# Performance work log

Measured on AMD Instinct MI355X. Metric: run time of the kernel, lower is better.

The kernel has to match this reference:

```python
import jax, jax.numpy as jnp
import numpy as np

B, N, IN_DIM, HEADS, PER_HEAD = 8, 512, 256, 4, 32
OUT_DIM = HEADS * PER_HEAD  # 128
NEG_SLOPE = 0.2


def setup_inputs() -> dict:
    key = jax.random.key(0)
    ks = jax.random.split(key, 8)
    x = jax.random.normal(ks[0], (B, N, IN_DIM), jnp.float32)
    adj = jax.random.randint(ks[1], (B, N, N), 0, 2, jnp.int32)
    sl = 1.0 / np.sqrt(IN_DIM)
    W_l = jax.random.normal(ks[2], (IN_DIM, OUT_DIM), jnp.float32) * sl  # source proj
    b_l = jnp.zeros((OUT_DIM,), jnp.float32)
    W_r = jax.random.normal(ks[3], (IN_DIM, OUT_DIM), jnp.float32) * sl  # target proj
    b_r = jnp.zeros((OUT_DIM,), jnp.float32)
    att = jax.random.normal(ks[4], (HEADS, PER_HEAD), jnp.float32) * (1.0 / np.sqrt(PER_HEAD))
    bias = jnp.zeros((OUT_DIM,), jnp.float32)
    return {"x": x, "adj": adj, "W_l": W_l, "b_l": b_l, "W_r": W_r, "b_r": b_r,
            "att": att, "bias": bias}


def _gatv2_single(x_b, adj_b, W_l, b_l, W_r, b_r, att, bias):
    # PyG GATv2Conv: remove_self_loops + add_self_loops -> diagonal forced to 1
    n = x_b.shape[0]
    adj_sl = jnp.fill_diagonal(adj_b, 1, inplace=False)
    # edge_index = adj.nonzero().t(): source = row, target = col
    m = (adj_sl != 0).T  # m[i, j]: source j feeds target i
    xl = (x_b @ W_l + b_l).reshape(n, HEADS, PER_HEAD)  # source-side features
    xr = (x_b @ W_r + b_r).reshape(n, HEADS, PER_HEAD)  # target-side features
    s = xr[:, None] + xl[None, :]                       # [i, j, H, C]
    s = jnp.where(s > 0, s, NEG_SLOPE * s)              # LeakyReLU(0.2)
    e = jnp.einsum('ijhc,hc->ijh', s, att)              # attention logits
    e = jnp.where(m[..., None], e, -jnp.inf)
    alpha = jax.nn.softmax(e, axis=1)                   # softmax over sources j
    out = jnp.einsum('ijh,jhc->ihc', alpha, xl).reshape(n, HEADS * PER_HEAD)
    return out + bias


def reference(x, adj, W_l, b_l, W_r, b_r, att, bias):
    # Sequential per-batch processing, faithful to the original Python loop
    # and keeping the [N,N,H,C] intermediate to one graph at a time.
    def one(args):
        x_b, adj_b = args
        return _gatv2_single(x_b, adj_b, W_l, b_l, W_r, b_r, att, bias)
    return jax.lax.map(one, (x, adj))  # [B, N, OUT_DIM]
```

## Files before the change

### kernel.cpp

```cpp
#include <hip/hip_runtime.h>
#include <hip/hip_bf16.h>

#define B_   8
#define N_   512
#define IND  256
#define H_   4
#define PH   32
#define OD   128
#define TI   4

typedef float v2f __attribute__((ext_vector_type(2)));

#define ATT_SCALE 0.5770780163555854f
#define DLR_SCALE 0.8656170245333781f

template <int PAT>
__device__ __forceinline__ float dpp_add(float x) {
    int yi = __builtin_amdgcn_mov_dpp(__float_as_int(x), PAT, 0xF, 0xF, true);
    return x + __int_as_float(yi);
}

__device__ __forceinline__ float fast_exp2(float x) {
#if __has_builtin(__builtin_amdgcn_exp2f)
    return __builtin_amdgcn_exp2f(x);
#else
    return exp2f(x);
#endif
}

__device__ __forceinline__ void pk_fma(v2f& d, v2f a, v2f b) {
    asm("v_pk_fma_f32 %0, %1, %2, %0" : "+v"(d) : "v"(a), "v"(b));
}

__global__ __launch_bounds__(256, 2) void proj_kernel(
    const float* __restrict__ x,
    const float* __restrict__ Wl, const float* __restrict__ bl,
    const float* __restrict__ Wr, const float* __restrict__ br,
    const float* __restrict__ att,
    float* __restrict__ xl, float* __restrict__ xr,
    float* __restrict__ dl, float* __restrict__ dr)
{
    __shared__ float xs[8 * IND];
    const int t = threadIdx.x;
    const int row0 = blockIdx.x * 8;

    const float4* xp4 = (const float4*)(x + (size_t)row0 * IND);
    float4* xs4 = (float4*)xs;
    #pragma unroll
    for (int k = 0; k < 2; ++k)
        xs4[t + k * 256] = xp4[t + k * 256];
    __syncthreads();

    const int which = t >> 7;
    const int rg = (t >> 6) & 1;
    const int og = t & 63;
    const int o0 = og * 2;
    const int r0 = rg * 4;
    const float* W  = which ? Wr : Wl;
    const float* bb = which ? br : bl;

    float acc0[4], acc1[4];
    #pragma unroll
    for (int r = 0; r < 4; ++r) { acc0[r] = 0.f; acc1[r] = 0.f; }

    for (int k = 0; k < IND; k += 4) {
        float wf0[4], wf1[4];
        #pragma unroll
        for (int kk = 0; kk < 4; ++kk) {
            float2 wv = *(const float2*)(W + (size_t)(k + kk) * OD + o0);
            wf0[kk] = wv.x;
            wf1[kk] = wv.y;
        }
        float xv[4][4];
        #pragma unroll
        for (int r = 0; r < 4; ++r)
            *(float4*)(xv[r]) = *(const float4*)(&xs[(r0 + r) * IND + k]);
        #pragma unroll
        for (int kk = 0; kk < 4; ++kk)
            #pragma unroll
            for (int r = 0; r < 4; ++r) {
                acc0[r] = fmaf(xv[r][kk], wf0[kk], acc0[r]);
                acc1[r] = fmaf(xv[r][kk], wf1[kk], acc1[r]);
            }
    }

    const float bv0 = bb[o0];
    const float bv1 = bb[o0 + 1];
    const float a0 = att[o0];
    const float a1 = att[o0 + 1];
    float* dst = which ? xr : xl;
    float* dp  = which ? dr : dl;
    float dcon[4];
    #pragma unroll
    for (int r = 0; r < 4; ++r) {
        float y0 = acc0[r] + bv0;
        float y1 = acc1[r] + bv1;
        *(float2*)(&dst[(size_t)(row0 + r0 + r) * OD + o0]) = make_float2(y0, y1);
        dcon[r] = fmaf(a0, y0, a1 * y1);
    }
    #pragma unroll
    for (int m = 1; m < 16; m <<= 1) {
        #pragma unroll
        for (int r = 0; r < 4; ++r)
            dcon[r] += __shfl_xor(dcon[r], m);
    }
    if ((og & 15) == 0) {
        const int h = og >> 4;
        #pragma unroll
        for (int r = 0; r < 4; ++r)
            dp[(size_t)(row0 + r0 + r) * H_ + h] = DLR_SCALE * dcon[r];
    }
}

__global__ __launch_bounds__(256, 3) void attn_kernel(
    const int* __restrict__ adj, const float* __restrict__ att,
    const float* __restrict__ bias,
    const float* __restrict__ xl, const float* __restrict__ xr,
    const float* __restrict__ dl, const float* __restrict__ dr,
    float* __restrict__ out)
{
    __shared__ float sacc[H_][16][TI][PH];
    __shared__ float ssum[H_][16][TI];

    const int t = threadIdx.x;
    const int b  = blockIdx.x >> 7;
    const int i0 = (blockIdx.x & 127) * TI;
    const int cq = t & 3;
    const int js = (t >> 2) & 15;
    const int h  = t >> 6;
    const int cbase = h * PH + cq * 8;

    float atS[8];
    {
        const float* ap = att + cbase;
        float4 a0 = *(const float4*)(ap);
        float4 a1 = *(const float4*)(ap + 4);
        atS[0] = ATT_SCALE * a0.x; atS[1] = ATT_SCALE * a0.y;
        atS[2] = ATT_SCALE * a0.z; atS[3] = ATT_SCALE * a0.w;
        atS[4] = ATT_SCALE * a1.x; atS[5] = ATT_SCALE * a1.y;
        atS[6] = ATT_SCALE * a1.z; atS[7] = ATT_SCALE * a1.w;
    }
    float xrS[TI][8];
    float drv[TI];
    #pragma unroll
    for (int il = 0; il < TI; ++il) {
        const float* xp = xr + ((size_t)(b * N_ + i0 + il)) * OD + cbase;
        float4 r0 = *(const float4*)(xp);
        float4 r1 = *(const float4*)(xp + 4);
        xrS[il][0] = r0.x; xrS[il][1] = r0.y; xrS[il][2] = r0.z; xrS[il][3] = r0.w;
        xrS[il][4] = r1.x; xrS[il][5] = r1.y; xrS[il][6] = r1.z; xrS[il][7] = r1.w;
        drv[il] = dr[((size_t)(b * N_ + i0 + il)) * H_ + h];
    }

    v2f acc[TI][4];
    float sumw[TI];
    #pragma unroll
    for (int il = 0; il < TI; ++il) {
        sumw[il] = 0.f;
        #pragma unroll
        for (int m = 0; m < 4; ++m) acc[il][m] = (v2f){0.f, 0.f};
    }

    const float* xlp = xl + ((size_t)(b * N_ + js)) * OD + cbase;
    const int*   ajp = adj + ((size_t)(b * N_ + js)) * N_ + i0;
    const float* dlp = dl + ((size_t)(b * N_ + js)) * H_ + h;

    float4 va = *(const float4*)(xlp);
    float4 vb = *(const float4*)(xlp + 4);
    int4   mj = *(const int4*)(ajp);
    float  dj = *dlp;

    #pragma unroll 2
    for (int u = 0; u < 32; ++u) {
        float4 wa = va, wb = vb;
        int4   wm = mj;
        float  wd = dj;
        if (u < 31) {
            xlp += 16 * OD; ajp += 16 * N_; dlp += 16 * H_;
            va = *(const float4*)(xlp);
            vb = *(const float4*)(xlp + 4);
            mj = *(const int4*)(ajp);
            dj = *dlp;
        }
        const int j = u * 16 + js;
        v2f p0 = (v2f){wa.x, wa.y}, p1 = (v2f){wa.z, wa.w};
        v2f p2 = (v2f){wb.x, wb.y}, p3 = (v2f){wb.z, wb.w};
        int wmv[4] = {wm.x, wm.y, wm.z, wm.w};
        #pragma unroll
        for (int il = 0; il < TI; ++il) {
            float s, e2a = 0.f, e2b = 0.f;
            s = xrS[il][0] + wa.x; e2a = fmaf(atS[0], __builtin_fabsf(s), e2a);
            s = xrS[il][1] + wa.y; e2b = fmaf(atS[1], __builtin_fabsf(s), e2b);
            s = xrS[il][2] + wa.z; e2a = fmaf(atS[2], __builtin_fabsf(s), e2a);
            s = xrS[il][3] + wa.w; e2b = fmaf(atS[3], __builtin_fabsf(s), e2b);
            s = xrS[il][4] + wb.x; e2a = fmaf(atS[4], __builtin_fabsf(s), e2a);
            s = xrS[il][5] + wb.y; e2b = fmaf(atS[5], __builtin_fabsf(s), e2b);
            s = xrS[il][6] + wb.z; e2a = fmaf(atS[6], __builtin_fabsf(s), e2a);
            s = xrS[il][7] + wb.w; e2b = fmaf(atS[7], __builtin_fabsf(s), e2b);
            float eh = e2a + e2b;
            eh = dpp_add<0xB1>(eh);
            eh = dpp_add<0x4E>(eh);
            float e = (wd + drv[il]) + eh;
            bool keep = (wmv[il] != 0) || (j == i0 + il);
            float w = keep ? fast_exp2(e) : 0.f;
            sumw[il] += w;
            v2f ws = (v2f){w, w};
            pk_fma(acc[il][0], ws, p0);
            pk_fma(acc[il][1], ws, p1);
            pk_fma(acc[il][2], ws, p2);
            pk_fma(acc[il][3], ws, p3);
        }
    }

    #pragma unroll
    for (int il = 0; il < TI; ++il) {
        float4 w0 = make_float4(acc[il][0].x, acc[il][0].y,
                                acc[il][1].x, acc[il][1].y);
        float4 w1 = make_float4(acc[il][2].x, acc[il][2].y,
                                acc[il][3].x, acc[il][3].y);
        *(float4*)(&sacc[h][js][il][cq * 8])     = w0;
        *(float4*)(&sacc[h][js][il][cq * 8 + 4]) = w1;
    }
    if (cq == 0) {
        #pragma unroll
        for (int il = 0; il < TI; ++il)
            ssum[h][js][il] = sumw[il];
    }
    __syncthreads();

    const int lane = t & 63;
    const int o = lane * 2;
    const int il2 = o >> 5;
    const int c2 = o & 31;
    float st = 0.f;
    #pragma unroll
    for (int k = 0; k < 16; ++k) st += ssum[h][k][il2];
    float a0 = 0.f, a1 = 0.f;
    #pragma unroll
    for (int k = 0; k < 16; ++k) {
        float2 p = *(const float2*)(&sacc[h][k][il2][c2]);
        a0 += p.x; a1 += p.y;
    }
    const float inv = 1.f / st;
    const int c = h * PH + c2;
    float* op = out + ((size_t)(b * N_ + i0 + il2)) * OD;
    *(float2*)(&op[c]) = make_float2(fmaf(a0, inv, bias[c]),
                                     fmaf(a1, inv, bias[c + 1]));
}

extern "C" void kernel_launch(void* const* d_in, const int* in_sizes, int n_in,
                              void* d_out, int out_size, void* d_ws, size_t ws_size,
                              hipStream_t stream) {
    const float* x    = (const float*)d_in[0];
    const int*   adj  = (const int*)d_in[1];
    const float* Wl   = (const float*)d_in[2];
    const float* bl   = (const float*)d_in[3];
    const float* Wr   = (const float*)d_in[4];
    const float* br   = (const float*)d_in[5];
    const float* att  = (const float*)d_in[6];
    const float* bias = (const float*)d_in[7];
    float* out = (float*)d_out;

    float* xl = (float*)d_ws;
    float* xr = xl + (size_t)B_ * N_ * OD;
    float* dl = xr + (size_t)B_ * N_ * OD;
    float* dr = dl + (size_t)B_ * N_ * H_;

    proj_kernel<<<512, 256, 0, stream>>>(x, Wl, bl, Wr, br, att, xl, xr, dl, dr);
    attn_kernel<<<1024, 256, 0, stream>>>(adj, att, bias, xl, xr, dl, dr, out);
}
```

Measured before the change: 121.2 us.

## Halve target tile and replace shared-memory reduction with shuffle transpose-reduce

The per-block target tile shrinks from four rows to two, so the grid doubles to 2048 blocks and each thread keeps fewer accumulators. The final cross-source reduction no longer goes through shared memory and a __syncthreads. It uses a butterfly transpose-reduce with __shfl_xor inside each wavefront, so each lane ends up owning one output element. This gives more parallelism and removes LDS traffic and the barrier, but each xl row and dl value is now reloaded for half as many targets, roughly doubling global and cache traffic for xl.

```diff
diff --git a/kernel.cpp b/kernel.cpp
--- a/kernel.cpp
+++ b/kernel.cpp
@@ -7,7 +7,7 @@
 #define H_   4
 #define PH   32
 #define OD   128
-#define TI   4
+#define TI   2
 
 typedef float v2f __attribute__((ext_vector_type(2)));
 
@@ -119,12 +119,9 @@
     const float* __restrict__ dl, const float* __restrict__ dr,
     float* __restrict__ out)
 {
-    __shared__ float sacc[H_][16][TI][PH];
-    __shared__ float ssum[H_][16][TI];
-
     const int t = threadIdx.x;
-    const int b  = blockIdx.x >> 7;
-    const int i0 = (blockIdx.x & 127) * TI;
+    const int b  = blockIdx.x >> 8;
+    const int i0 = (blockIdx.x & 255) * TI;
     const int cq = t & 3;
     const int js = (t >> 2) & 15;
     const int h  = t >> 6;
@@ -167,25 +164,25 @@
 
     float4 va = *(const float4*)(xlp);
     float4 vb = *(const float4*)(xlp + 4);
-    int4   mj = *(const int4*)(ajp);
+    int2   mj = *(const int2*)(ajp);
     float  dj = *dlp;
 
     #pragma unroll 2
     for (int u = 0; u < 32; ++u) {
         float4 wa = va, wb = vb;
-        int4   wm = mj;
+        int2   wm = mj;
         float  wd = dj;
         if (u < 31) {
             xlp += 16 * OD; ajp += 16 * N_; dlp += 16 * H_;
             va = *(const float4*)(xlp);
             vb = *(const float4*)(xlp + 4);
-            mj = *(const int4*)(ajp);
+            mj = *(const int2*)(ajp);
             dj = *dlp;
         }
         const int j = u * 16 + js;
         v2f p0 = (v2f){wa.x, wa.y}, p1 = (v2f){wa.z, wa.w};
         v2f p2 = (v2f){wb.x, wb.y}, p3 = (v2f){wb.z, wb.w};
-        int wmv[4] = {wm.x, wm.y, wm.z, wm.w};
+        int wmv[TI] = {wm.x, wm.y};
         #pragma unroll
         for (int il = 0; il < TI; ++il) {
             float s, e2a = 0.f, e2b = 0.f;
@@ -214,38 +211,64 @@
 
     #pragma unroll
     for (int il = 0; il < TI; ++il) {
-        float4 w0 = make_float4(acc[il][0].x, acc[il][0].y,
-                                acc[il][1].x, acc[il][1].y);
-        float4 w1 = make_float4(acc[il][2].x, acc[il][2].y,
-                                acc[il][3].x, acc[il][3].y);
-        *(float4*)(&sacc[h][js][il][cq * 8])     = w0;
-        *(float4*)(&sacc[h][js][il][cq * 8 + 4]) = w1;
-    }
-    if (cq == 0) {
-        #pragma unroll
-        for (int il = 0; il < TI; ++il)
-            ssum[h][js][il] = sumw[il];
-    }
-    __syncthreads();
-
-    const int lane = t & 63;
-    const int o = lane * 2;
-    const int il2 = o >> 5;
-    const int c2 = o & 31;
-    float st = 0.f;
-    #pragma unroll
-    for (int k = 0; k < 16; ++k) st += ssum[h][k][il2];
-    float a0 = 0.f, a1 = 0.f;
-    #pragma unroll
-    for (int k = 0; k < 16; ++k) {
-        float2 p = *(const float2*)(&sacc[h][k][il2][c2]);
-        a0 += p.x; a1 += p.y;
-    }
-    const float inv = 1.f / st;
-    const int c = h * PH + c2;
-    float* op = out + ((size_t)(b * N_ + i0 + il2)) * OD;
-    *(float2*)(&op[c]) = make_float2(fmaf(a0, inv, bias[c]),
-                                     fmaf(a1, inv, bias[c + 1]));
+        sumw[il] += __shfl_xor(sumw[il], 4);
+        sumw[il] += __shfl_xor(sumw[il], 8);
+        sumw[il] += __shfl_xor(sumw[il], 16);
+        sumw[il] += __shfl_xor(sumw[il], 32);
+    }
+
+    float accf[16];
+    #pragma unroll
+    for (int il = 0; il < TI; ++il)
+        #pragma unroll
+        for (int m = 0; m < 4; ++m) {
+            accf[il * 8 + 2 * m]     = acc[il][m].x;
+            accf[il * 8 + 2 * m + 1] = acc[il][m].y;
+        }
+
+    float r8[8];
+    {
+        const bool hi = (js & 1) != 0;
+        #pragma unroll
+        for (int m = 0; m < 8; ++m) {
+            float send = hi ? accf[m] : accf[8 + m];
+            float keep = hi ? accf[8 + m] : accf[m];
+            r8[m] = keep + __shfl_xor(send, 4);
+        }
+    }
+    float r4[4];
+    {
+        const bool hi = (js & 2) != 0;
+        #pragma unroll
+        for (int m = 0; m < 4; ++m) {
+            float send = hi ? r8[m] : r8[4 + m];
+            float keep = hi ? r8[4 + m] : r8[m];
+            r4[m] = keep + __shfl_xor(send, 8);
+        }
+    }
+    float r2[2];
+    {
+        const bool hi = (js & 4) != 0;
+        #pragma unroll
+        for (int m = 0; m < 2; ++m) {
+            float send = hi ? r4[m] : r4[2 + m];
+            float keep = hi ? r4[2 + m] : r4[m];
+            r2[m] = keep + __shfl_xor(send, 16);
+        }
+    }
+    float r1;
+    {
+        const bool hi = (js & 8) != 0;
+        float send = hi ? r2[0] : r2[1];
+        float keep = hi ? r2[1] : r2[0];
+        r1 = keep + __shfl_xor(send, 32);
+    }
+
+    const int il = js & 1;
+    const int coff = ((js >> 1) & 1) * 4 + ((js >> 2) & 1) * 2 + ((js >> 3) & 1);
+    const int c = cbase + coff;
+    const float inv = 1.f / sumw[il];
+    out[((size_t)(b * N_ + i0 + il)) * OD + c] = fmaf(r1, inv, bias[c]);
 }
 
 extern "C" void kernel_launch(void* const* d_in, const int* in_sizes, int n_in,
@@ -267,5 +290,5 @@
     float* dr = dl + (size_t)B_ * N_ * H_;
 
     proj_kernel<<<512, 256, 0, stream>>>(x, Wl, bl, Wr, br, att, xl, xr, dl, dr);
-    attn_kernel<<<1024, 256, 0, stream>>>(adj, att, bias, xl, xr, dl, dr, out);
-}
+    attn_kernel<<<2048, 256, 0, stream>>>(adj, att, bias, xl, xr, dl, dr, out);
+}
```

Result: slower. 130.4 us (+7.6%).
